# Kernel optimization log

Measured on AMD Instinct MI355X. Metric: run time of the kernel, lower is better.

Reference implementation:

```python
import jax, jax.numpy as jnp
import numpy as np

B, LQ, D, H, NL, NP, DFF = 8, 1800, 256, 8, 4, 4, 1024
DH = D // H
SHAPES = np.array([[100, 150], [50, 75], [25, 38], [13, 19]], dtype=np.int64)
LIN = int((SHAPES[:, 0] * SHAPES[:, 1]).sum())
QN, QP = -8.0, 7.0  # 4-bit signed LSQ


def lsq(w, alpha):
    """LSQ weight quantization (per-tensor scale, STE round/grad-scale)."""
    g = 1.0 / jnp.sqrt(w.size * QP)
    a = alpha * g + jax.lax.stop_gradient(alpha - alpha * g)  # grad-scaled alpha
    wn = jnp.clip(w / a, QN, QP)
    wq = wn + jax.lax.stop_gradient(jnp.round(wn) - wn)       # round with STE
    return wq * a


def linear_q(x, w, b, a):
    return x @ lsq(w, a).T + b


def layer_norm(x, g, b, eps=1e-5):
    m = x.mean(-1, keepdims=True)
    v = ((x - m) ** 2).mean(-1, keepdims=True)
    return (x - m) / jnp.sqrt(v + eps) * g + b


def setup_inputs():
    key = jax.random.key(0)
    ks = list(jax.random.split(key, 20))

    def nrm(i, shape, s=0.02):
        return jax.random.normal(ks[i], shape, jnp.float32) * s

    def alpha(w):
        return 2.0 * jnp.mean(jnp.abs(w)) / jnp.sqrt(QP)

    qW, kW, vW, oW = nrm(0, (D, D)), nrm(1, (D, D)), nrm(2, (D, D)), nrm(3, (D, D))
    val_W = nrm(4, (D, D))
    off_W = nrm(5, (H * NL * NP * 2, D))
    aw_W = nrm(6, (H * NL * NP, D))
    out_W = nrm(7, (D, D))
    W1, W2 = nrm(8, (DFF, D)), nrm(9, (D, DFF))
    lsi = np.concatenate([[0], np.cumsum(SHAPES[:, 0] * SHAPES[:, 1])[:-1]]).astype(np.int64)
    z = jnp.zeros
    return dict(
        tgt=nrm(10, (B, LQ, D), 1.0),
        query_pos=nrm(11, (B, LQ, D), 1.0),
        reference_points=jax.random.uniform(ks[12], (B, LQ, NL, 2), jnp.float32),
        src=nrm(13, (B, LIN, D), 1.0),
        qW=qW, qb=z(D), kW=kW, kb=z(D), vW=vW, vb=z(D), oW=oW, ob=z(D),
        a_q=alpha(qW), a_k=alpha(kW), a_v=alpha(vW), a_o=alpha(oW),
        val_W=val_W, val_b=z(D), a_val=alpha(val_W),
        off_W=off_W, off_b=z(H * NL * NP * 2),
        aw_W=aw_W, aw_b=z(H * NL * NP),
        out_W=out_W, out_b=z(D), a_out=alpha(out_W),
        W1=W1, b1=z(DFF), a_w1=alpha(W1),
        W2=W2, b2=z(D), a_w2=alpha(W2),
        ln1_g=jnp.ones(D), ln1_b=z(D),
        ln2_g=jnp.ones(D), ln2_b=z(D),
        ln3_g=jnp.ones(D), ln3_b=z(D),
        src_spatial_shapes=jnp.asarray(SHAPES),
        level_start_index=jnp.asarray(lsi),
        src_padding_mask=jnp.zeros((B, LIN), dtype=bool),
    )


def reference(tgt, query_pos, reference_points, src,
              qW, qb, kW, kb, vW, vb, oW, ob, a_q, a_k, a_v, a_o,
              val_W, val_b, a_val, off_W, off_b, aw_W, aw_b, out_W, out_b, a_out,
              W1, b1, a_w1, W2, b2, a_w2,
              ln1_g, ln1_b, ln2_g, ln2_b, ln3_g, ln3_b,
              src_spatial_shapes, level_start_index, src_padding_mask):
    shapes = np.asarray(src_spatial_shapes)  # static spatial shapes per level

    # ---- quantized self-attention (dropout = eval mode, i.e. identity) ----
    qk_in = tgt + query_pos
    q = linear_q(qk_in, qW, qb, a_q).reshape(B, LQ, H, DH)
    k = linear_q(qk_in, kW, kb, a_k).reshape(B, LQ, H, DH)
    v = linear_q(tgt, vW, vb, a_v).reshape(B, LQ, H, DH)
    scores = jnp.einsum('bqhd,bkhd->bhqk', q, k) / jnp.sqrt(jnp.float32(DH))
    p = jax.nn.softmax(scores, axis=-1)
    sa = jnp.einsum('bhqk,bkhd->bqhd', p, v).reshape(B, LQ, D)
    tgt = layer_norm(tgt + linear_q(sa, oW, ob, a_o), ln2_g, ln2_b)

    # ---- quantized multi-scale deformable cross-attention ----
    query = tgt + query_pos
    value = linear_q(src, val_W, val_b, a_val)
    value = jnp.where(src_padding_mask[..., None], 0.0, value)
    value = value.reshape(B, LIN, H, DH)
    offs = (query @ off_W.T + off_b).reshape(B, LQ, H, NL, NP, 2)
    aw = (query @ aw_W.T + aw_b).reshape(B, LQ, H, NL * NP)
    aw = jax.nn.softmax(aw, axis=-1).reshape(B, LQ, H, NL, NP)
    # offset normalizer is (W_l, H_l)
    norm = jnp.asarray(shapes[:, ::-1].astype(np.float32))  # [NL, 2]
    loc = reference_points[:, :, None, :, None, :] + offs / norm[None, None, None, :, None, :]

    bidx = jnp.arange(B)[:, None, None, None]
    hidx = jnp.arange(H)[None, None, :, None]
    acc = jnp.zeros((B, LQ, H, DH), jnp.float32)
    start = 0
    for l in range(NL):
        Hl, Wl = int(shapes[l, 0]), int(shapes[l, 1])
        v_l = jax.lax.dynamic_slice_in_dim(value, start, Hl * Wl, 1).reshape(B, Hl, Wl, H, DH)
        # grid_sample semantics: align_corners=False, zero padding
        x = loc[:, :, :, l, :, 0] * Wl - 0.5  # [B, LQ, H, NP]
        y = loc[:, :, :, l, :, 1] * Hl - 0.5
        x0 = jnp.floor(x); y0 = jnp.floor(y)
        x0i = x0.astype(jnp.int32); y0i = y0.astype(jnp.int32)
        wx1 = x - x0; wy1 = y - y0
        wx0 = 1.0 - wx1; wy0 = 1.0 - wy1

        def gather(yi, xi):
            valid = (yi >= 0) & (yi < Hl) & (xi >= 0) & (xi < Wl)
            yc = jnp.clip(yi, 0, Hl - 1); xc = jnp.clip(xi, 0, Wl - 1)
            g = v_l[bidx, yc, xc, hidx]  # [B, LQ, H, NP, DH]
            return g * valid[..., None]

        samp = (gather(y0i, x0i) * (wy0 * wx0)[..., None]
                + gather(y0i, x0i + 1) * (wy0 * wx1)[..., None]
                + gather(y0i + 1, x0i) * (wy1 * wx0)[..., None]
                + gather(y0i + 1, x0i + 1) * (wy1 * wx1)[..., None])
        acc = acc + (aw[:, :, :, l, :, None] * samp).sum(axis=3)
        start += Hl * Wl

    ca = linear_q(acc.reshape(B, LQ, D), out_W, out_b, a_out)
    tgt = layer_norm(tgt + ca, ln1_g, ln1_b)

    # ---- quantized FFN ----
    t2 = linear_q(jax.nn.relu(linear_q(tgt, W1, b1, a_w1)), W2, b2, a_w2)
    tgt = layer_norm(tgt + t2, ln3_g, ln3_b)
    return tgt
```

## Files before the change

### kernel.cpp

```cpp
#include <hip/hip_runtime.h>
#include <hip/hip_bf16.h>

static constexpr int B_   = 8;
static constexpr int LQ_  = 1800;
static constexpr int D_   = 256;
static constexpr int H_   = 8;
static constexpr int DFF_ = 1024;
static constexpr int LIN_ = 19947;
static constexpr int MQ_  = B_ * LQ_;
static constexpr int NELEM_ = MQ_ * D_;
static constexpr int PREPN_ = 1016704;

#define CDIV(a, b) (((a) + (b) - 1) / (b))

typedef unsigned short u16;
typedef unsigned int   u32;
typedef unsigned long long u64;
typedef __attribute__((ext_vector_type(8))) __bf16 bf16x8;
typedef __attribute__((ext_vector_type(4))) float  f32x4;
typedef __attribute__((ext_vector_type(4))) u32    u32x4;

#if __has_builtin(__builtin_amdgcn_exp2f)
#define EXP2(x) __builtin_amdgcn_exp2f(x)
#else
#define EXP2(x) exp2f(x)
#endif

__device__ __forceinline__ u16 f2bf(float f) {
    union { __bf16 h; u16 u; } v; v.h = (__bf16)f; return v.u;
}
__device__ __forceinline__ float bf2f(u16 u) {
    union { u32 u; float f; } v; v.u = ((u32)u) << 16;
    return v.f;
}

__device__ __forceinline__ f32x4 mfma_bf16(bf16x8 a, bf16x8 b, f32x4 c) {
    return __builtin_amdgcn_mfma_f32_16x16x32_bf16(a, b, c, 0, 0, 0);
}

__device__ __forceinline__ void gload16(const void* g, void* l) {
    __builtin_amdgcn_global_load_lds(
        (const __attribute__((address_space(1))) void*)g,
        (__attribute__((address_space(3))) void*)l,
        16, 0, 0);
}

template <int N> __device__ __forceinline__ void waitvm() {
    if constexpr (N == 0) asm volatile("s_waitcnt vmcnt(0)" ::: "memory");
    else if constexpr (N == 3) asm volatile("s_waitcnt vmcnt(3)" ::: "memory");
    else if constexpr (N == 4) asm volatile("s_waitcnt vmcnt(4)" ::: "memory");
    else if constexpr (N == 6) asm volatile("s_waitcnt vmcnt(6)" ::: "memory");
}
__device__ __forceinline__ void cfence() { asm volatile("" ::: "memory"); }

__device__ __forceinline__ void storey(float* p, float v) { *p = v; }
__device__ __forceinline__ void storey(u16* p, float v)   { *p = f2bf(v); }

__global__ void k_prep(
    const float* __restrict__ qW,   const float* __restrict__ kW,
    const float* __restrict__ vW,   const float* __restrict__ oW,
    const float* __restrict__ valW, const float* __restrict__ outW,
    const float* __restrict__ W1,   const float* __restrict__ W2,
    const float* __restrict__ offW, const float* __restrict__ awW,
    const float* __restrict__ a_q,  const float* __restrict__ a_k,
    const float* __restrict__ a_v,  const float* __restrict__ a_o,
    const float* __restrict__ a_val,const float* __restrict__ a_out,
    const float* __restrict__ a_w1, const float* __restrict__ a_w2,
    const float* __restrict__ qb,   const float* __restrict__ kb,
    const float* __restrict__ off_b,const float* __restrict__ aw_b,
    const float* __restrict__ tgt,  const float* __restrict__ qpos,
    u16* __restrict__ wout, float* __restrict__ bout,
    u16* __restrict__ A, u16* __restrict__ Bb)
{
    int i = blockIdx.x * 256 + threadIdx.x;
    auto q8 = [&](const float* w, const float* al, int off) {
        float a = al[0];
        float wn = fminf(fmaxf(w[off] / a, -8.f), 7.f);
        wout[i] = f2bf(rintf(wn) * a);
    };
    if      (i <   65536) q8(qW,   a_q,   i);
    else if (i <  131072) q8(kW,   a_k,   i -   65536);
    else if (i <  196608) q8(vW,   a_v,   i -  131072);
    else if (i <  262144) q8(oW,   a_o,   i -  196608);
    else if (i <  327680) q8(valW, a_val, i -  262144);
    else if (i <  393216) q8(outW, a_out, i -  327680);
    else if (i <  655360) q8(W1,   a_w1,  i -  393216);
    else if (i <  917504) q8(W2,   a_w2,  i -  655360);
    else if (i <  983040) wout[i] = f2bf(offW[i - 917504]);
    else if (i < 1015808) wout[i] = f2bf(awW[i - 983040]);
    else if (i < 1016320) { int j = i - 1015808; bout[j]       = (j < 256) ? qb[j]    : kb[j - 256];  }
    else if (i < PREPN_)  { int j = i - 1016320; bout[512 + j] = (j < 256) ? off_b[j] : aw_b[j - 256]; }
    else {
        int j = i - PREPN_;
        if (j < NELEM_) { float t = tgt[j]; A[j] = f2bf(t + qpos[j]); Bb[j] = f2bf(t); }
    }
}

template <typename XT, typename OT, bool RELU, int BN, bool PAIR>
__global__ __launch_bounds__(256) void k_gemm3(
    const XT* __restrict__ X, const u16* __restrict__ W,
    const float* __restrict__ bias, OT* __restrict__ Y,
    int M, int N, int K)
{
    constexpr int WN  = BN / 2;
    constexpr int NFR = WN / 16;
    constexpr bool XF32 = (sizeof(XT) == 4);
    constexpr int L = (XF32 ? 2 : 1) + BN / 64;
    constexpr int ASZ = 64 * 32 * (XF32 ? 2 : 1);
    constexpr int BSZ = BN * 32;
    __shared__ __align__(16) u16 As[2][ASZ];
    __shared__ __align__(16) u16 Bs[2][BSZ];

    const int tid = threadIdx.x;
    const int wave = tid >> 6, lane = tid & 63;
    const int wr = wave >> 1, wc = wave & 1;
    const int fr = lane & 15, fg = lane >> 4;
    int bm, bn;
    if constexpr (PAIR) { bm = (blockIdx.x >> 1) * 64; bn = (blockIdx.x & 1) * BN; }
    else                { bm = blockIdx.x * 64;        bn = blockIdx.y * BN; }

    f32x4 acc[2][NFR];
    #pragma unroll
    for (int m = 0; m < 2; ++m)
        #pragma unroll
        for (int n = 0; n < NFR; ++n) acc[m][n] = (f32x4){0.f, 0.f, 0.f, 0.f};

    auto stageA = [&](int buf, int kt) {
        if constexpr (!XF32) {
            int r = (wave << 4) + (lane >> 2);
            int grow = bm + r; if (grow > M - 1) grow = M - 1;
            int cs = (lane & 3) ^ ((lane >> 3) & 3);
            gload16((const u16*)X + (size_t)grow * K + (kt << 5) + (cs << 3),
                    &As[buf][wave * 512]);
        } else {
            float* Af = (float*)As[buf];
            #pragma unroll
            for (int t = 0; t < 2; ++t) {
                int r = (t << 5) + (wave << 3) + (lane >> 3);
                int grow = bm + r; if (grow > M - 1) grow = M - 1;
                int cs = (lane & 7) ^ ((lane >> 3) & 7);
                gload16((const float*)X + (size_t)grow * K + (kt << 5) + (cs << 2),
                        &Af[((t << 5) + (wave << 3)) * 32]);
            }
        }
    };
    auto stageB = [&](int buf, int kt) {
        #pragma unroll
        for (int t = 0; t < BN / 64; ++t) {
            int r = (t << 6) + (wave << 4) + (lane >> 2);
            int cs = (lane & 3) ^ ((lane >> 3) & 3);
            gload16(W + (size_t)(bn + r) * K + (kt << 5) + (cs << 3),
                    &Bs[buf][((t << 6) + (wave << 4)) * 32]);
        }
    };

    stageA(0, 0); stageB(0, 0);
    cfence();

    const int nk = K >> 5;
    int cur = 0;
    for (int kt = 0; kt < nk; ++kt) {
        if (kt + 1 < nk) {
            stageA(cur ^ 1, kt + 1); stageB(cur ^ 1, kt + 1);
            waitvm<L>();
        } else {
            waitvm<0>();
        }
        __builtin_amdgcn_s_barrier();

        bf16x8 af[2], bg[NFR];
        #pragma unroll
        for (int m = 0; m < 2; ++m) {
            int r = wr * 32 + m * 16 + fr;
            if constexpr (!XF32) {
                af[m] = *(const bf16x8*)&As[cur][r * 32 + ((fg ^ ((fr >> 1) & 3)) << 3)];
            } else {
                const float* Af = (const float*)As[cur];
                int s0 = (fg << 1) ^ (fr & 7);
                f32x4 x0 = *(const f32x4*)&Af[r * 32 + (s0 << 2)];
                f32x4 x1 = *(const f32x4*)&Af[r * 32 + ((s0 ^ 1) << 2)];
                #pragma unroll
                for (int j = 0; j < 4; ++j) {
                    af[m][j]     = (__bf16)x0[j];
                    af[m][4 + j] = (__bf16)x1[j];
                }
            }
        }
        #pragma unroll
        for (int n = 0; n < NFR; ++n) {
            int r = wc * WN + n * 16 + fr;
            bg[n] = *(const bf16x8*)&Bs[cur][r * 32 + ((fg ^ ((fr >> 1) & 3)) << 3)];
        }
        #pragma unroll
        for (int m = 0; m < 2; ++m)
            #pragma unroll
            for (int n = 0; n < NFR; ++n)
                acc[m][n] = mfma_bf16(af[m], bg[n], acc[m][n]);

        __builtin_amdgcn_s_barrier();
        cur ^= 1;
    }

    #pragma unroll
    for (int m = 0; m < 2; ++m) {
        #pragma unroll
        for (int i = 0; i < 4; ++i) {
            int grow = bm + wr * 32 + m * 16 + fg * 4 + i;
            if (grow >= M) continue;
            #pragma unroll
            for (int n = 0; n < NFR; ++n) {
                int gcol = bn + wc * WN + n * 16 + fr;
                float v = acc[m][n][i] + bias[gcol];
                if (RELU) v = fmaxf(v, 0.f);
                storey(Y + (size_t)grow * N + gcol, v);
            }
        }
    }
}

__global__ __launch_bounds__(256) void k_attn(
    const u16* __restrict__ QK, const u16* __restrict__ V, u16* __restrict__ O)
{
    __shared__ u16 Ks[128 * 40];
    __shared__ u16 Vt[32 * 136];
    const int b = blockIdx.z, h = blockIdx.y;
    const int q0 = blockIdx.x * 64;
    const int tid = threadIdx.x;
    const int wave = tid >> 6, lane = tid & 63;
    const int fr = lane & 15, fg = lane >> 4;
    constexpr float C2 = 0.25503486f;

    int qg = q0 + wave * 16 + fr; if (qg >= LQ_) qg = LQ_ - 1;
    bf16x8 qf;
    {
        bf16x8 qraw = *(const bf16x8*)&QK[((size_t)(b * LQ_ + qg)) * 512 + h * 32 + fg * 8];
        #pragma unroll
        for (int j = 0; j < 8; ++j) qf[j] = (__bf16)((float)qraw[j] * C2);
    }

    const bf16x8 ones = {(__bf16)1.f, (__bf16)1.f, (__bf16)1.f, (__bf16)1.f,
                         (__bf16)1.f, (__bf16)1.f, (__bf16)1.f, (__bf16)1.f};

    f32x4 o0 = (f32x4){0.f,0.f,0.f,0.f}, o1 = (f32x4){0.f,0.f,0.f,0.f};
    f32x4 lacc = (f32x4){0.f,0.f,0.f,0.f};

    const int kr = tid >> 1, kc = (tid & 1) * 16;
    const int vp = lane, vdh = wave * 8;
    const int cp = ((vp >> 4) << 4) | (((vp >> 1) & 3) << 2) | (((vp >> 3) & 1) << 1) | (vp & 1);

    for (int kb0 = 0; kb0 < LQ_; kb0 += 128) {
        const bool tail = (kb0 + 128 > LQ_);
        __syncthreads();
        {
            int kg = kb0 + kr; if (kg >= LQ_) kg = LQ_ - 1;
            const u16* kp = &QK[((size_t)(b * LQ_ + kg)) * 512 + 256 + h * 32 + kc];
            *(bf16x8*)&Ks[kr * 40 + kc]     = *(const bf16x8*)kp;
            *(bf16x8*)&Ks[kr * 40 + kc + 8] = *(const bf16x8*)(kp + 8);
            int v0 = kb0 + 2 * vp, v1 = v0 + 1;
            if (v0 >= LQ_) v0 = LQ_ - 1;
            if (v1 >= LQ_) v1 = LQ_ - 1;
            union { bf16x8 v; u16 s[8]; } va, vb2;
            va.v  = *(const bf16x8*)&V[((size_t)(b * LQ_ + v0)) * 256 + h * 32 + vdh];
            vb2.v = *(const bf16x8*)&V[((size_t)(b * LQ_ + v1)) * 256 + h * 32 + vdh];
            #pragma unroll
            for (int j = 0; j < 8; ++j)
                *(u32*)&Vt[(vdh + j) * 136 + 2 * cp] = (u32)va.s[j] | ((u32)vb2.s[j] << 16);
        }
        __syncthreads();

        u32x4 pq[4];
        #pragma unroll
        for (int f = 0; f < 8; ++f) {
            bf16x8 ka = *(const bf16x8*)&Ks[(f * 16 + fr) * 40 + fg * 8];
            f32x4 s = mfma_bf16(ka, qf, (f32x4){0.f,0.f,0.f,0.f});
            if (tail) {
                #pragma unroll
                for (int i = 0; i < 4; ++i)
                    if (kb0 + f * 16 + fg * 4 + i >= LQ_) s[i] = -3e38f;
            }
            float p0 = EXP2(s[0]), p1 = EXP2(s[1]);
            float p2 = EXP2(s[2]), p3 = EXP2(s[3]);
            union { __bf16 h[2]; u32 w; } c0, c1;
            c0.h[0] = (__bf16)p0; c0.h[1] = (__bf16)p1;
            c1.h[0] = (__bf16)p2; c1.h[1] = (__bf16)p3;
            pq[f >> 1][(f & 1) * 2 + 0] = c0.w;
            pq[f >> 1][(f & 1) * 2 + 1] = c1.w;
        }

        __builtin_amdgcn_s_setprio(1);
        #pragma unroll
        for (int ks = 0; ks < 4; ++ks) {
            bf16x8 pb  = __builtin_bit_cast(bf16x8, pq[ks]);
            bf16x8 va0 = *(const bf16x8*)&Vt[fr * 136 + ks * 32 + fg * 8];
            bf16x8 va1 = *(const bf16x8*)&Vt[(16 + fr) * 136 + ks * 32 + fg * 8];
            o0 = mfma_bf16(va0, pb, o0);
            o1 = mfma_bf16(va1, pb, o1);
            lacc = mfma_bf16(ones, pb, lacc);
        }
        __builtin_amdgcn_s_setprio(0);
    }

    float inv = 1.f / lacc[0];
    int qout = q0 + wave * 16 + fr;
    if (qout < LQ_) {
        size_t base = ((size_t)(b * LQ_ + qout)) * 256 + h * 32;
        #pragma unroll
        for (int i = 0; i < 4; ++i) {
            O[base + fg * 4 + i]      = f2bf(o0[i] * inv);
            O[base + 16 + fg * 4 + i] = f2bf(o1[i] * inv);
        }
    }
}

__device__ __forceinline__ float ldf(const float* p) { return *p; }
__device__ __forceinline__ float ldf(const u16* p)   { return bf2f(*p); }

template <typename RT, typename OT>
__global__ __launch_bounds__(256) void k_resln(
    const u16* __restrict__ X, const RT* __restrict__ R,
    const float* __restrict__ g, const float* __restrict__ bb,
    OT* __restrict__ O)
{
    const int row = blockIdx.x;
    const int d = threadIdx.x;
    const size_t off = (size_t)row * D_ + d;
    float v = ldf(R + off) + bf2f(X[off]);
    __shared__ float r1[4], r2[4];
    int lane = d & 63, wid = d >> 6;
    float s = v;
    #pragma unroll
    for (int o_ = 32; o_ >= 1; o_ >>= 1) s += __shfl_xor(s, o_);
    if (lane == 0) r1[wid] = s;
    __syncthreads();
    float mean = (r1[0] + r1[1] + r1[2] + r1[3]) * (1.f / 256.f);
    float dv = v - mean;
    float sq = dv * dv;
    #pragma unroll
    for (int o_ = 32; o_ >= 1; o_ >>= 1) sq += __shfl_xor(sq, o_);
    if (lane == 0) r2[wid] = sq;
    __syncthreads();
    float var = (r2[0] + r2[1] + r2[2] + r2[3]) * (1.f / 256.f);
    storey(O + off, dv / sqrtf(var + 1e-5f) * g[d] + bb[d]);
}

template <typename RT>
__global__ __launch_bounds__(256) void k_resln2(
    const u16* __restrict__ X, const RT* __restrict__ R,
    const float* __restrict__ g, const float* __restrict__ bb,
    const float* __restrict__ qpos,
    u16* __restrict__ O1, u16* __restrict__ O2)
{
    const int row = blockIdx.x;
    const int d = threadIdx.x;
    const size_t off = (size_t)row * D_ + d;
    float v = ldf(R + off) + bf2f(X[off]);
    __shared__ float r1[4], r2[4];
    int lane = d & 63, wid = d >> 6;
    float s = v;
    #pragma unroll
    for (int o_ = 32; o_ >= 1; o_ >>= 1) s += __shfl_xor(s, o_);
    if (lane == 0) r1[wid] = s;
    __syncthreads();
    float mean = (r1[0] + r1[1] + r1[2] + r1[3]) * (1.f / 256.f);
    float dv = v - mean;
    float sq = dv * dv;
    #pragma unroll
    for (int o_ = 32; o_ >= 1; o_ >>= 1) sq += __shfl_xor(sq, o_);
    if (lane == 0) r2[wid] = sq;
    __syncthreads();
    float var = (r2[0] + r2[1] + r2[2] + r2[3]) * (1.f / 256.f);
    float y = dv / sqrtf(var + 1e-5f) * g[d] + bb[d];
    O1[off] = f2bf(y);
    O2[off] = f2bf(y + qpos[off]);
}

__global__ __launch_bounds__(256) void k_sample(
    const float* __restrict__ oaw,
    const u16* __restrict__ value, const float* __restrict__ refp,
    u16* __restrict__ acc_out)
{
    __shared__ __align__(16) u32 pts[4][128][8];
    const int t = threadIdx.x;
    const int bq0 = blockIdx.x * 4;
    const int b = bq0 / LQ_;

    constexpr int Hl[4] = {100, 50, 25, 13};
    constexpr int Wl[4] = {150, 75, 38, 19};
    constexpr int LS[4] = {0, 15000, 18750, 19700};

    #pragma unroll
    for (int j = 0; j < 2; ++j) {
        const int gidx = t + j * 256;
        const int qsub = gidx >> 7;
        const int pt = gidx & 127;
        const int h = pt >> 4, lp = pt & 15;
        const int l = lp >> 2, p = lp & 3;
        const int bq = bq0 + qsub;

        float2 oxy = *(const float2*)&oaw[(size_t)bq * 384 + h * 32 + l * 8 + p * 2];
        float av = oaw[(size_t)bq * 384 + 256 + h * 16 + lp];
        float mx = av;
        #pragma unroll
        for (int s = 1; s < 16; s <<= 1) mx = fmaxf(mx, __shfl_xor(mx, s));
        float e = __expf(av - mx);
        float sum = e;
        #pragma unroll
        for (int s = 1; s < 16; s <<= 1) sum += __shfl_xor(sum, s);
        float a = e / sum;

        float2 rxy = *(const float2*)&refp[(size_t)bq * 8 + l * 2];
        const float Wf = (float)Wl[l], Hf = (float)Hl[l];
        float x = (rxy.x + oxy.x / Wf) * Wf - 0.5f;
        float y = (rxy.y + oxy.y / Hf) * Hf - 0.5f;
        float x0f = floorf(x), y0f = floorf(y);
        int x0 = (int)x0f, y0 = (int)y0f;
        float wx1 = x - x0f, wy1 = y - y0f;
        float wx0 = 1.f - wx1, wy0 = 1.f - wy1;

        u32 ov[4]; float wv[4];
        #pragma unroll
        for (int c = 0; c < 4; ++c) {
            int cy = c >> 1, cx = c & 1;
            int yi = y0 + cy, xi = x0 + cx;
            bool valid = (yi >= 0) && (yi < Hl[l]) && (xi >= 0) && (xi < Wl[l]);
            ov[c] = valid ? (u32)((LS[l] + yi * Wl[l] + xi) * 256 + h * 32) : 0u;
            float w = (cy ? wy1 : wy0) * (cx ? wx1 : wx0) * a;
            wv[c] = valid ? w : 0.f;
        }
        u32* dst = pts[qsub][lp * 8 + h];
        *(uint4*)dst = make_uint4(ov[0], ov[1], ov[2], ov[3]);
        float4 wq = make_float4(wv[0], wv[1], wv[2], wv[3]);
        *(float4*)(dst + 4) = wq;
    }
    __syncthreads();

    const int qsub = t >> 6;
    const int rem = t & 63;
    const int h = rem >> 3;
    const int dq = rem & 7;
    const u16* vb = value + (size_t)b * LIN_ * 256 + 4 * dq;
    float a0 = 0.f, a1 = 0.f, a2 = 0.f, a3 = 0.f;
    #pragma unroll
    for (int i = 0; i < 16; ++i) {
        const u32* P = pts[qsub][i * 8 + h];
        uint4 o4 = *(const uint4*)P;
        float4 w4 = *(const float4*)(P + 4);
        u64 g;
        g = *(const u64*)&vb[o4.x];
        a0 += w4.x * bf2f((u16)g);         a1 += w4.x * bf2f((u16)(g >> 16));
        a2 += w4.x * bf2f((u16)(g >> 32)); a3 += w4.x * bf2f((u16)(g >> 48));
        g = *(const u64*)&vb[o4.y];
        a0 += w4.y * bf2f((u16)g);         a1 += w4.y * bf2f((u16)(g >> 16));
        a2 += w4.y * bf2f((u16)(g >> 32)); a3 += w4.y * bf2f((u16)(g >> 48));
        g = *(const u64*)&vb[o4.z];
        a0 += w4.z * bf2f((u16)g);         a1 += w4.z * bf2f((u16)(g >> 16));
        a2 += w4.z * bf2f((u16)(g >> 32)); a3 += w4.z * bf2f((u16)(g >> 48));
        g = *(const u64*)&vb[o4.w];
        a0 += w4.w * bf2f((u16)g);         a1 += w4.w * bf2f((u16)(g >> 16));
        a2 += w4.w * bf2f((u16)(g >> 32)); a3 += w4.w * bf2f((u16)(g >> 48));
    }
    const int bq = bq0 + qsub;
    u64 packed = (u64)f2bf(a0) | ((u64)f2bf(a1) << 16)
               | ((u64)f2bf(a2) << 32) | ((u64)f2bf(a3) << 48);
    *(u64*)&acc_out[(size_t)bq * 256 + h * 32 + 4 * dq] = packed;
}

extern "C" void kernel_launch(void* const* d_in, const int* in_sizes, int n_in,
                              void* d_out, int out_size, void* d_ws, size_t ws_size,
                              hipStream_t stream)
{
    (void)in_sizes; (void)n_in; (void)out_size; (void)ws_size;
    const float* tgt   = (const float*)d_in[0];
    const float* qpos  = (const float*)d_in[1];
    const float* refp  = (const float*)d_in[2];
    const float* src   = (const float*)d_in[3];
    const float* qW    = (const float*)d_in[4];
    const float* qb    = (const float*)d_in[5];
    const float* kW    = (const float*)d_in[6];
    const float* kb    = (const float*)d_in[7];
    const float* vW    = (const float*)d_in[8];
    const float* vb    = (const float*)d_in[9];
    const float* oW    = (const float*)d_in[10];
    const float* ob    = (const float*)d_in[11];
    const float* a_q   = (const float*)d_in[12];
    const float* a_k   = (const float*)d_in[13];
    const float* a_v   = (const float*)d_in[14];
    const float* a_o   = (const float*)d_in[15];
    const float* val_W = (const float*)d_in[16];
    const float* val_b = (const float*)d_in[17];
    const float* a_val = (const float*)d_in[18];
    const float* off_W = (const float*)d_in[19];
    const float* off_b = (const float*)d_in[20];
    const float* aw_W  = (const float*)d_in[21];
    const float* aw_b  = (const float*)d_in[22];
    const float* out_W = (const float*)d_in[23];
    const float* out_b = (const float*)d_in[24];
    const float* a_out = (const float*)d_in[25];
    const float* W1    = (const float*)d_in[26];
    const float* b1    = (const float*)d_in[27];
    const float* a_w1  = (const float*)d_in[28];
    const float* W2    = (const float*)d_in[29];
    const float* b2    = (const float*)d_in[30];
    const float* a_w2  = (const float*)d_in[31];
    const float* ln1_g = (const float*)d_in[32];
    const float* ln1_b = (const float*)d_in[33];
    const float* ln2_g = (const float*)d_in[34];
    const float* ln2_b = (const float*)d_in[35];
    const float* ln3_g = (const float*)d_in[36];
    const float* ln3_b = (const float*)d_in[37];

    u16* wbase = (u16*)d_ws;
    u16* wq_q  = wbase;
    u16* wq_v  = wbase + 131072;
    u16* wq_o  = wbase + 196608;
    u16* wq_vl = wbase + 262144;
    u16* wq_ot = wbase + 327680;
    u16* wq_1  = wbase + 393216;
    u16* wq_2  = wbase + 655360;
    u16* w_off = wbase + 917504;
    float* bfused = (float*)(wbase + 1015808);
    u16* bufA = (u16*)(bfused + 1024);
    u16* bufB = bufA + NELEM_;
    u16* bufC = bufB + NELEM_;
    u16* bufD = bufC + NELEM_;
    u16* bufE = bufD + NELEM_;
    float* oaw = (float*)(bufE + NELEM_);
    u16* valb  = (u16*)(oaw + (size_t)MQ_ * 384);

    const int TB = 256;
    const int MVAL = B_ * LIN_;
    const int GM = MQ_ / 64;
    const int GV = CDIV(MVAL, 64);

    k_prep<<<CDIV(PREPN_ + NELEM_, TB), TB, 0, stream>>>(
        qW, kW, vW, oW, val_W, out_W, W1, W2, off_W, aw_W,
        a_q, a_k, a_v, a_o, a_val, a_out, a_w1, a_w2,
        qb, kb, off_b, aw_b, tgt, qpos, wbase, bfused, bufA, bufB);

    k_gemm3<u16, u16, false, 128, false><<<dim3(GM, 4), TB, 0, stream>>>(bufA, wq_q, bfused, bufC, MQ_, 512, 256);
    k_gemm3<u16, u16, false, 128, false><<<dim3(GM, 2), TB, 0, stream>>>(bufB, wq_v, vb, bufE, MQ_, 256, 256);
    k_attn<<<dim3(CDIV(LQ_,64), H_, B_), TB, 0, stream>>>(bufC, bufE, bufA);
    k_gemm3<u16, u16, false, 128, false><<<dim3(GM, 2), TB, 0, stream>>>(bufA, wq_o, ob, bufD, MQ_, 256, 256);
    k_resln2<float><<<MQ_, TB, 0, stream>>>(bufD, tgt, ln2_g, ln2_b, qpos, bufC, bufD);

    k_gemm3<float, u16, false, 128, true><<<dim3(GV * 2, 1), TB, 0, stream>>>(src, wq_vl, val_b, valb, MVAL, 256, 256);
    k_gemm3<u16, float, false, 128, false><<<dim3(GM, 3), TB, 0, stream>>>(bufD, w_off, bfused + 512, oaw, MQ_, 384, 256);
    k_sample<<<MQ_ / 4, TB, 0, stream>>>(oaw, valb, refp, bufE);
    k_gemm3<u16, u16, false, 128, false><<<dim3(GM, 2), TB, 0, stream>>>(bufE, wq_ot, out_b, bufA, MQ_, 256, 256);
    k_resln<u16, u16><<<MQ_, TB, 0, stream>>>(bufA, bufC, ln1_g, ln1_b, bufB);

    u16* ffn1 = valb;
    k_gemm3<u16, u16, true , 128, false><<<dim3(GM, 8), TB, 0, stream>>>(bufB, wq_1, b1, ffn1, MQ_, 1024, 256);
    k_gemm3<u16, u16, false, 128, false><<<dim3(GM, 2), TB, 0, stream>>>(ffn1, wq_2, b2, bufD, MQ_, 256, 1024);
    k_resln<u16, float><<<MQ_, TB, 0, stream>>>(bufD, bufB, ln3_g, ln3_b, (float*)d_out);
}
```

Measured before the change: 355.8 us.

## Merge independent value, QK and V projection GEMMs into one interleaved launch

The value projection of src and the Q/K and V projections of the self-attention are merged into a single kernel. Its blocks interleave the three GEMMs (two value tiles per one QK/V tile), so the independent work shares the GPU and launch gaps are removed. The value GEMM now uses 256-wide N tiles instead of the paired 128-wide tiles, and GEMM shared memory becomes a dynamic-sized buffer passed into a device body. Risks are a larger shared-memory footprint (48KB per block), lower occupancy for all fused blocks, and load imbalance between the f32-input and bf16-input tiles.

```diff
diff --git a/kernel.cpp b/kernel.cpp
--- a/kernel.cpp
+++ b/kernel.cpp
@@ -10,6 +10,11 @@
 static constexpr int MQ_  = B_ * LQ_;
 static constexpr int NELEM_ = MQ_ * D_;
 static constexpr int PREPN_ = 1016704;
+static constexpr int MVAL_ = B_ * LIN_;
+static constexpr int GM_   = MQ_ / 64;
+static constexpr int GVAL_ = (MVAL_ + 63) / 64;
+static constexpr int GOTH_ = GM_ * 4 + GM_ * 2;
+static constexpr int GFUSED_ = 3 * GOTH_;
 
 #define CDIV(a, b) (((a) + (b) - 1) / (b))
 
@@ -96,11 +101,11 @@
     }
 }
 
-template <typename XT, typename OT, bool RELU, int BN, bool PAIR>
-__global__ __launch_bounds__(256) void k_gemm3(
+template <typename XT, typename OT, bool RELU, int BN>
+__device__ __forceinline__ void gemm_body(
     const XT* __restrict__ X, const u16* __restrict__ W,
     const float* __restrict__ bias, OT* __restrict__ Y,
-    int M, int N, int K)
+    int M, int N, int K, int bxi, int byi, u16* smem)
 {
     constexpr int WN  = BN / 2;
     constexpr int NFR = WN / 16;
@@ -108,16 +113,14 @@
     constexpr int L = (XF32 ? 2 : 1) + BN / 64;
     constexpr int ASZ = 64 * 32 * (XF32 ? 2 : 1);
     constexpr int BSZ = BN * 32;
-    __shared__ __align__(16) u16 As[2][ASZ];
-    __shared__ __align__(16) u16 Bs[2][BSZ];
+    u16* As[2] = { smem, smem + ASZ };
+    u16* Bs[2] = { smem + 2 * ASZ, smem + 2 * ASZ + BSZ };
 
     const int tid = threadIdx.x;
     const int wave = tid >> 6, lane = tid & 63;
     const int wr = wave >> 1, wc = wave & 1;
     const int fr = lane & 15, fg = lane >> 4;
-    int bm, bn;
-    if constexpr (PAIR) { bm = (blockIdx.x >> 1) * 64; bn = (blockIdx.x & 1) * BN; }
-    else                { bm = blockIdx.x * 64;        bn = blockIdx.y * BN; }
+    const int bm = bxi * 64, bn = byi * BN;
 
     f32x4 acc[2][NFR];
     #pragma unroll
@@ -214,6 +217,46 @@
                 if (RELU) v = fmaxf(v, 0.f);
                 storey(Y + (size_t)grow * N + gcol, v);
             }
+        }
+    }
+}
+
+template <typename XT, typename OT, bool RELU, int BN>
+__global__ __launch_bounds__(256) void k_gemm3(
+    const XT* __restrict__ X, const u16* __restrict__ W,
+    const float* __restrict__ bias, OT* __restrict__ Y,
+    int M, int N, int K)
+{
+    constexpr int SM = 2 * (64 * 32 * (sizeof(XT) == 4 ? 2 : 1) + BN * 32);
+    __shared__ __align__(16) u16 smem[SM];
+    gemm_body<XT, OT, RELU, BN>(X, W, bias, Y, M, N, K, blockIdx.x, blockIdx.y, smem);
+}
+
+__global__ __launch_bounds__(256) void k_gemm_fused(
+    const float* __restrict__ src,  const u16* __restrict__ wq_vl,
+    const float* __restrict__ val_b,u16* __restrict__ valb,
+    const u16* __restrict__ bufA,   const u16* __restrict__ wq_q,
+    const float* __restrict__ qkb,  u16* __restrict__ bufC,
+    const u16* __restrict__ bufB,   const u16* __restrict__ wq_v,
+    const float* __restrict__ vbias,u16* __restrict__ bufE)
+{
+    __shared__ __align__(16) u16 smem[24576];
+    const int ix = blockIdx.x;
+    const int r = ix % 3;
+    if (r != 2) {
+        int v = (ix / 3) * 2 + r;
+        if (v >= GVAL_) return;
+        gemm_body<float, u16, false, 256>(src, wq_vl, val_b, valb,
+                                          MVAL_, 256, 256, v, 0, smem);
+    } else {
+        int o = ix / 3;
+        if (o < GM_ * 4) {
+            gemm_body<u16, u16, false, 128>(bufA, wq_q, qkb, bufC,
+                                            MQ_, 512, 256, o % GM_, o / GM_, smem);
+        } else {
+            o -= GM_ * 4;
+            gemm_body<u16, u16, false, 128>(bufB, wq_v, vbias, bufE,
+                                            MQ_, 256, 256, o % GM_, o / GM_, smem);
         }
     }
 }
@@ -528,29 +571,28 @@
     u16* valb  = (u16*)(oaw + (size_t)MQ_ * 384);
 
     const int TB = 256;
-    const int MVAL = B_ * LIN_;
-    const int GM = MQ_ / 64;
-    const int GV = CDIV(MVAL, 64);
 
     k_prep<<<CDIV(PREPN_ + NELEM_, TB), TB, 0, stream>>>(
         qW, kW, vW, oW, val_W, out_W, W1, W2, off_W, aw_W,
         a_q, a_k, a_v, a_o, a_val, a_out, a_w1, a_w2,
         qb, kb, off_b, aw_b, tgt, qpos, wbase, bfused, bufA, bufB);
 
-    k_gemm3<u16, u16, false, 128, false><<<dim3(GM, 4), TB, 0, stream>>>(bufA, wq_q, bfused, bufC, MQ_, 512, 256);
-    k_gemm3<u16, u16, false, 128, false><<<dim3(GM, 2), TB, 0, stream>>>(bufB, wq_v, vb, bufE, MQ_, 256, 256);
+    k_gemm_fused<<<GFUSED_, TB, 0, stream>>>(
+        src, wq_vl, val_b, valb,
+        bufA, wq_q, bfused, bufC,
+        bufB, wq_v, vb, bufE);
+
     k_attn<<<dim3(CDIV(LQ_,64), H_, B_), TB, 0, stream>>>(bufC, bufE, bufA);
-    k_gemm3<u16, u16, false, 128, false><<<dim3(GM, 2), TB, 0, stream>>>(bufA, wq_o, ob, bufD, MQ_, 256, 256);
+    k_gemm3<u16, u16, false, 128><<<dim3(GM_, 2), TB, 0, stream>>>(bufA, wq_o, ob, bufD, MQ_, 256, 256);
     k_resln2<float><<<MQ_, TB, 0, stream>>>(bufD, tgt, ln2_g, ln2_b, qpos, bufC, bufD);
 
-    k_gemm3<float, u16, false, 128, true><<<dim3(GV * 2, 1), TB, 0, stream>>>(src, wq_vl, val_b, valb, MVAL, 256, 256);
-    k_gemm3<u16, float, false, 128, false><<<dim3(GM, 3), TB, 0, stream>>>(bufD, w_off, bfused + 512, oaw, MQ_, 384, 256);
+    k_gemm3<u16, float, false, 128><<<dim3(GM_, 3), TB, 0, stream>>>(bufD, w_off, bfused + 512, oaw, MQ_, 384, 256);
     k_sample<<<MQ_ / 4, TB, 0, stream>>>(oaw, valb, refp, bufE);
-    k_gemm3<u16, u16, false, 128, false><<<dim3(GM, 2), TB, 0, stream>>>(bufE, wq_ot, out_b, bufA, MQ_, 256, 256);
+    k_gemm3<u16, u16, false, 128><<<dim3(GM_, 2), TB, 0, stream>>>(bufE, wq_ot, out_b, bufA, MQ_, 256, 256);
     k_resln<u16, u16><<<MQ_, TB, 0, stream>>>(bufA, bufC, ln1_g, ln1_b, bufB);
 
     u16* ffn1 = valb;
-    k_gemm3<u16, u16, true , 128, false><<<dim3(GM, 8), TB, 0, stream>>>(bufB, wq_1, b1, ffn1, MQ_, 1024, 256);
-    k_gemm3<u16, u16, false, 128, false><<<dim3(GM, 2), TB, 0, stream>>>(ffn1, wq_2, b2, bufD, MQ_, 256, 1024);
+    k_gemm3<u16, u16, true , 128><<<dim3(GM_, 8), TB, 0, stream>>>(bufB, wq_1, b1, ffn1, MQ_, 1024, 256);
+    k_gemm3<u16, u16, false, 128><<<dim3(GM_, 2), TB, 0, stream>>>(ffn1, wq_2, b2, bufD, MQ_, 256, 1024);
     k_resln<u16, float><<<MQ_, TB, 0, stream>>>(bufD, bufB, ln3_g, ln3_b, (float*)d_out);
 }
```

Result: faster. 344.3 us (-3.2%).
